# Optimization experiments

Hardware: AMD Instinct MI355X
Metric: run time of the kernel (lower is better)

Reference implementation:

```python
import jax, jax.numpy as jnp
import numpy as np

B, L, D, H = 2, 4096, 1024, 1  # head_dim == embed_dim in source, forcing H=1


def setup_inputs() -> dict:
    key = jax.random.key(0)
    k_x, kq, kk, kv, ko = jax.random.split(key, 5)
    s = 1.0 / np.sqrt(D)
    return {
        "x": jax.random.normal(k_x, (B, L, D), dtype=jnp.float32),
        "W_q": jax.random.normal(kq, (D, D), dtype=jnp.float32) * s,
        "W_k": jax.random.normal(kk, (D, D), dtype=jnp.float32) * s,
        "W_v": jax.random.normal(kv, (D, D), dtype=jnp.float32) * s,
        "W_o": jax.random.normal(ko, (D, D), dtype=jnp.float32) * s,
    }


def reference(x, W_q, W_k, W_v, W_o):
    # nn.Linear(y) = y @ W.T ; weights stored as (out, in)
    Hd = D  # head_dim = embed_dim (source quirk), so num_heads must be 1
    Q = jnp.einsum('bld,ed->ble', x, W_q).reshape(B, L, H, Hd).transpose(0, 2, 1, 3)
    K = jnp.einsum('bld,ed->ble', x, W_k).reshape(B, L, H, Hd).transpose(0, 2, 1, 3)
    V = jnp.einsum('bld,ed->ble', x, W_v).reshape(B, L, H, Hd).transpose(0, 2, 1, 3)
    scores = jnp.einsum('bhqd,bhkd->bhqk', Q, K) / jnp.sqrt(jnp.float32(Hd))
    attn = jax.nn.softmax(scores, axis=-1)
    out = jnp.einsum('bhqk,bhkd->bhqd', attn, V)  # (B,H,L,Hd)
    out = out.transpose(0, 2, 1, 3).reshape(B, L, D)
    return jnp.einsum('bld,ed->ble', out, W_o)
```

## Files before the change

### kernel.cpp

```cpp
#include <hip/hip_runtime.h>
#include <hip/hip_bf16.h>
#include <stdint.h>


typedef unsigned short u16;
typedef short short8 __attribute__((ext_vector_type(8)));
typedef float f32x4 __attribute__((ext_vector_type(4)));

__device__ __forceinline__ void async_ld16(void* lds, const void* g) {
  __builtin_amdgcn_global_load_lds(
      (const __attribute__((address_space(1))) unsigned int*)g,
      (__attribute__((address_space(3))) unsigned int*)lds,
      16, 0, 0);
}

__device__ __forceinline__ u16 f2bf(float f) {
  unsigned u = __float_as_uint(f);
  u += 0x7FFFu + ((u >> 16) & 1u);
  return (u16)(u >> 16);
}

__global__ __launch_bounds__(256)
void cast_f32_bf16(const float* __restrict__ in, u16* __restrict__ out, int n) {
  const int i = (blockIdx.x * 256 + threadIdx.x) * 8;
  if (i >= n) return;
  float4 a = ((const float4*)(in + i))[0];
  float4 b = ((const float4*)(in + i))[1];
  uint4 o;
  o.x = (unsigned)f2bf(a.x) | ((unsigned)f2bf(a.y) << 16);
  o.y = (unsigned)f2bf(a.z) | ((unsigned)f2bf(a.w) << 16);
  o.z = (unsigned)f2bf(b.x) | ((unsigned)f2bf(b.y) << 16);
  o.w = (unsigned)f2bf(b.z) | ((unsigned)f2bf(b.w) << 16);
  *(uint4*)(out + i) = o;
}

__global__ __launch_bounds__(256)
void cast_w4_bf16(const float* __restrict__ w0, const float* __restrict__ w1,
                  const float* __restrict__ w2, const float* __restrict__ w3,
                  u16* __restrict__ out) {
  const int idx = (blockIdx.x * 256 + threadIdx.x) * 8;
  const int which = idx >> 20;
  const int off = idx & 1048575;
  const float* src = which == 0 ? w0 : which == 1 ? w1 : which == 2 ? w2 : w3;
  float4 a = ((const float4*)(src + off))[0];
  float4 b = ((const float4*)(src + off))[1];
  uint4 o;
  o.x = (unsigned)f2bf(a.x) | ((unsigned)f2bf(a.y) << 16);
  o.y = (unsigned)f2bf(a.z) | ((unsigned)f2bf(a.w) << 16);
  o.z = (unsigned)f2bf(b.x) | ((unsigned)f2bf(b.y) << 16);
  o.w = (unsigned)f2bf(b.z) | ((unsigned)f2bf(b.w) << 16);
  *(uint4*)(out + idx) = o;
}

#define BM 128
#define BN 128
#define BK 32

template <int XSWZ>
__global__ __launch_bounds__(256)
void gemm_bt(const u16* __restrict__ A, const u16* __restrict__ Bt,
             void* __restrict__ Cv, int K, int lda, int ldb, int ldc,
             long long sAz, long long sBz, long long sCz,
             float scale, int store_f32) {
  __shared__ u16 As[3][BM * BK];
  __shared__ u16 Bs[3][BN * BK];

  int bx, by, bz;
  if constexpr (XSWZ) {
    const int gx = gridDim.x, gy = gridDim.y;
    const int nwg = gx * gy * gridDim.z;
    const int lin = (blockIdx.z * gy + blockIdx.y) * gx + blockIdx.x;
    const int chunk = nwg >> 3;
    const int swz = (lin & 7) * chunk + (lin >> 3);
    bx = swz % gx;
    const int t1 = swz / gx;
    by = t1 % gy;
    bz = t1 / gy;
  } else {
    bx = blockIdx.x; by = blockIdx.y; bz = blockIdx.z;
  }

  A  += (long long)bz * sAz;
  Bt += (long long)bz * sBz;

  const int tid  = threadIdx.x;
  const int wave = tid >> 6;
  const int lane = tid & 63;
  const int wm   = wave >> 1;
  const int wn   = wave & 1;
  const int r15  = lane & 15;
  const int q4   = lane >> 4;

  const int tileM = by * BM;
  const int tileN = bx * BN;

  const int srow = tid >> 2;
  const int scol = ((tid & 3) ^ (srow & 3)) * 8;

  const u16* Aptr = A + (long long)tileM * lda + scol;
  const u16* Bptr = Bt + (long long)tileN * ldb + scol;

  auto stage = [&](int kt) {
    const int b = kt % 3;
    const int k0 = kt * BK;
    u16* as = &As[b][tid * 8];
    u16* bs = &Bs[b][tid * 8];
    async_ld16(as,        Aptr + (long long)srow * lda + k0);
    async_ld16(as + 2048, Aptr + (long long)(srow + 64) * lda + k0);
    async_ld16(bs,        Bptr + (long long)srow * ldb + k0);
    async_ld16(bs + 2048, Bptr + (long long)(srow + 64) * ldb + k0);
  };

  f32x4 zero = {0.f, 0.f, 0.f, 0.f};
  f32x4 acc[4][4];
#pragma unroll
  for (int i = 0; i < 4; ++i)
#pragma unroll
    for (int j = 0; j < 4; ++j) acc[i][j] = zero;

  const int csw = ((q4 ^ (r15 & 3)) * 8);

  const int NT = K / BK;
  stage(0);
  if (NT > 1) stage(1);
  if (NT > 2) stage(2);

  for (int kt = 0; kt < NT; ++kt) {
    const int rem = NT - 1 - kt;
    if (rem >= 2)      asm volatile("s_waitcnt vmcnt(8)" ::: "memory");
    else if (rem == 1) asm volatile("s_waitcnt vmcnt(4)" ::: "memory");
    else               asm volatile("s_waitcnt vmcnt(0)" ::: "memory");
    __builtin_amdgcn_s_barrier();

    const int b = kt % 3;
    const u16* as = &As[b][0];
    const u16* bs = &Bs[b][0];

    short8 af[4], bf[4];
#pragma unroll
    for (int i = 0; i < 4; ++i)
      af[i] = *(const short8*)&as[(wm * 64 + i * 16 + r15) * BK + csw];
#pragma unroll
    for (int i = 0; i < 4; ++i)
      bf[i] = *(const short8*)&bs[(wn * 64 + i * 16 + r15) * BK + csw];

    __builtin_amdgcn_s_setprio(1);
#pragma unroll
    for (int i = 0; i < 4; ++i)
#pragma unroll
      for (int j = 0; j < 4; ++j)
        acc[i][j] = __builtin_amdgcn_mfma_f32_16x16x32_bf16(af[i], bf[j], acc[i][j], 0, 0, 0);
    __builtin_amdgcn_s_setprio(0);

    __builtin_amdgcn_s_barrier();
    if (kt + 3 < NT) stage(kt + 3);
  }

#pragma unroll
  for (int i = 0; i < 4; ++i) {
#pragma unroll
    for (int j = 0; j < 4; ++j) {
      const int col = tileN + wn * 64 + j * 16 + r15;
#pragma unroll
      for (int r = 0; r < 4; ++r) {
        const int row = tileM + wm * 64 + i * 16 + q4 * 4 + r;
        const long long idx = (long long)bz * sCz + (long long)row * ldc + col;
        const float val = acc[i][j][r] * scale;
        if (store_f32) ((float*)Cv)[idx] = val;
        else           ((u16*)Cv)[idx] = f2bf(val);
      }
    }
  }
}

__global__ __launch_bounds__(512, 2)
void gemm256_8ph(const u16* __restrict__ A, const u16* __restrict__ Bt,
                 u16* __restrict__ C, int K, int lda, int ldb, int ldc,
                 long long sAz, long long sBz, long long sCz, float scale) {
  __shared__ u16 smem[49152];

  const int gx = gridDim.x, gy = gridDim.y;
  const int nwg = gx * gy * gridDim.z;
  const int lin = (blockIdx.z * gy + blockIdx.y) * gx + blockIdx.x;
  const int chunk = nwg >> 3;
  const int swz = (lin & 7) * chunk + (lin >> 3);
  const int bx = swz % gx;
  const int t1 = swz / gx;
  const int by = t1 % gy;
  const int bz = t1 / gy;

  A  += (long long)bz * sAz;
  Bt += (long long)bz * sBz;
  const long long cbase = (long long)bz * sCz;

  const int tid  = threadIdx.x;
  const int wid  = tid >> 6;
  const int lane = tid & 63;
  const int wm   = wid >> 2;
  const int wn   = wid & 3;
  const int r15  = lane & 15;
  const int q4   = lane >> 4;

  const int tileM = by * 256;
  const int tileN = bx * 256;

  const int sr  = tid >> 2;
  const int gc8 = ((((tid & 3) - ((tid >> 3) & 3)) & 3)) * 8;

  const u16* Asrc = A  + (long long)(tileM + sr) * lda + gc8;
  const u16* Bsrc = Bt + (long long)(tileN + sr) * ldb + gc8;

  auto stage2A = [&](int kt) {
    u16* d = &smem[(kt % 3) * 16384 + tid * 8];
    async_ld16(d,        Asrc + kt * 32);
    async_ld16(d + 4096, Asrc + (long long)128 * lda + kt * 32);
  };
  auto stage2B = [&](int kt) {
    u16* d = &smem[(kt % 3) * 16384 + 8192 + tid * 8];
    async_ld16(d,        Bsrc + kt * 32);
    async_ld16(d + 4096, Bsrc + (long long)128 * ldb + kt * 32);
  };

  const int csw = (((q4 + (r15 >> 1)) & 3)) * 8;

  f32x4 acc[8][4];
#pragma unroll
  for (int i = 0; i < 8; ++i)
#pragma unroll
    for (int j = 0; j < 4; ++j) acc[i][j] = (f32x4){0.f, 0.f, 0.f, 0.f};

  const int NT = K >> 5;

  stage2A(0); stage2B(0);
  if (NT > 1) { stage2A(1); stage2B(1); }

  for (int t = 0; t < NT; ++t) {
    if (t + 1 < NT) asm volatile("s_waitcnt vmcnt(4)" ::: "memory");
    else            asm volatile("s_waitcnt vmcnt(0)" ::: "memory");
    __builtin_amdgcn_s_barrier();

    const u16* bufA = &smem[(t % 3) * 16384];
    const u16* bufB = bufA + 8192;

    short8 bf[4], af[4];
#pragma unroll
    for (int j = 0; j < 4; ++j)
      bf[j] = *(const short8*)&bufB[(wn * 64 + j * 16 + r15) * 32 + csw];
#pragma unroll
    for (int i = 0; i < 4; ++i)
      af[i] = *(const short8*)&bufA[(wm * 128 + i * 16 + r15) * 32 + csw];
    if (t + 2 < NT) stage2A(t + 2);
    __builtin_amdgcn_s_barrier();

    __builtin_amdgcn_s_setprio(1);
#pragma unroll
    for (int i = 0; i < 4; ++i)
#pragma unroll
      for (int j = 0; j < 4; ++j)
        acc[i][j] = __builtin_amdgcn_mfma_f32_16x16x32_bf16(af[i], bf[j], acc[i][j], 0, 0, 0);
    __builtin_amdgcn_s_setprio(0);
    __builtin_amdgcn_s_barrier();

#pragma unroll
    for (int i = 0; i < 4; ++i)
      af[i] = *(const short8*)&bufA[(wm * 128 + 64 + i * 16 + r15) * 32 + csw];
    if (t + 2 < NT) stage2B(t + 2);
    __builtin_amdgcn_s_barrier();

    __builtin_amdgcn_s_setprio(1);
#pragma unroll
    for (int i = 0; i < 4; ++i)
#pragma unroll
      for (int j = 0; j < 4; ++j)
        acc[4 + i][j] = __builtin_amdgcn_mfma_f32_16x16x32_bf16(af[i], bf[j], acc[4 + i][j], 0, 0, 0);
    __builtin_amdgcn_s_setprio(0);
    __builtin_amdgcn_s_barrier();
  }

  const int crow = tileM + wm * 128 + q4 * 4;
  const int ccol = tileN + wn * 64 + r15;
#pragma unroll
  for (int mi = 0; mi < 8; ++mi)
#pragma unroll
    for (int nj = 0; nj < 4; ++nj)
#pragma unroll
      for (int r = 0; r < 4; ++r) {
        const long long row = crow + mi * 16 + r;
        C[cbase + row * ldc + (ccol + nj * 16)] = f2bf(acc[mi][nj][r] * scale);
      }
}

__global__ __launch_bounds__(256)
void softmax_rows(u16* __restrict__ S) {
  const int tid = threadIdx.x;
  u16* rp = S + (long long)blockIdx.x * 4096;

  uint4 a = ((const uint4*)rp)[tid * 2];
  uint4 b = ((const uint4*)rp)[tid * 2 + 1];
  unsigned w[8] = {a.x, a.y, a.z, a.w, b.x, b.y, b.z, b.w};
  float v[16];
#pragma unroll
  for (int i = 0; i < 8; ++i) {
    v[2 * i]     = __uint_as_float(w[i] << 16);
    v[2 * i + 1] = __uint_as_float(w[i] & 0xFFFF0000u);
  }

  float m = v[0];
#pragma unroll
  for (int i = 1; i < 16; ++i) m = fmaxf(m, v[i]);
#pragma unroll
  for (int o = 32; o > 0; o >>= 1) m = fmaxf(m, __shfl_xor(m, o));
  __shared__ float redm[4];
  __shared__ float reds[4];
  const int wave = tid >> 6;
  if ((tid & 63) == 0) redm[wave] = m;
  __syncthreads();
  m = fmaxf(fmaxf(redm[0], redm[1]), fmaxf(redm[2], redm[3]));

  float s = 0.f;
#pragma unroll
  for (int i = 0; i < 16; ++i) {
    v[i] = __expf(v[i] - m);
    s += v[i];
  }
#pragma unroll
  for (int o = 32; o > 0; o >>= 1) s += __shfl_xor(s, o);
  if ((tid & 63) == 0) reds[wave] = s;
  __syncthreads();
  s = (reds[0] + reds[1]) + (reds[2] + reds[3]);
  const float inv = 1.0f / s;

#pragma unroll
  for (int i = 0; i < 8; ++i)
    w[i] = (unsigned)f2bf(v[2 * i] * inv) | ((unsigned)f2bf(v[2 * i + 1] * inv) << 16);
  uint4 oa = {w[0], w[1], w[2], w[3]};
  uint4 ob = {w[4], w[5], w[6], w[7]};
  ((uint4*)rp)[tid * 2] = oa;
  ((uint4*)rp)[tid * 2 + 1] = ob;
}

extern "C" void kernel_launch(void* const* d_in, const int* in_sizes, int n_in,
                              void* d_out, int out_size, void* d_ws, size_t ws_size,
                              hipStream_t stream) {
  const float* x  = (const float*)d_in[0];
  const float* Wq = (const float*)d_in[1];
  const float* Wk = (const float*)d_in[2];
  const float* Wv = (const float*)d_in[3];
  const float* Wo = (const float*)d_in[4];
  float* out = (float*)d_out;

  u16* xb  = (u16*)d_ws;
  u16* Wqb = xb  + 8388608;
  u16* Wkb = Wqb + 1048576;
  u16* Wvb = Wkb + 1048576;
  u16* Wob = Wvb + 1048576;
  u16* QKp = Wob + 1048576;
  u16* Vt  = QKp + 16777216;
  u16* S   = Vt  + 8388608;
  u16* O   = QKp;

  const dim3 blk(256);

  cast_f32_bf16<<<dim3(4096), blk, 0, stream>>>(x, xb, 8388608);
  cast_w4_bf16<<<dim3(2048), blk, 0, stream>>>(Wq, Wk, Wv, Wo, Wqb);

  gemm_bt<1><<<dim3(16, 64, 1), blk, 0, stream>>>(xb, Wqb, QKp,
                                                  1024, 1024, 1024, 2048,
                                                  0, 0, 0, 1.f, 0);
  gemm_bt<0><<<dim3(64, 8, 1), blk, 0, stream>>>(Wvb, xb, Vt,
                                                 1024, 1024, 1024, 8192,
                                                 0, 0, 0, 1.f, 0);
  gemm256_8ph<<<dim3(16, 16, 2), dim3(512), 0, stream>>>(
      QKp, QKp + 1024, S, 1024, 2048, 2048, 4096,
      8388608LL, 8388608LL, 16777216LL, 0.03125f);
  softmax_rows<<<dim3(8192), blk, 0, stream>>>(S);
  gemm_bt<1><<<dim3(8, 32, 2), blk, 0, stream>>>(S, Vt, O,
                                                 4096, 4096, 8192, 1024,
                                                 16777216LL, 4096LL, 4194304LL,
                                                 1.f, 0);
  gemm_bt<1><<<dim3(8, 64, 1), blk, 0, stream>>>(O, Wob, out,
                                                 1024, 1024, 1024, 1024,
                                                 0, 0, 0, 1.f, 1);
}
```

Baseline: 389.8 us.

## Fuse softmax normalization into PV GEMM using precomputed row max and inverse sum

The softmax kernel now only computes per-row max and inverse sum, stored as float2 in reused workspace. The exponentiation is applied to the score tiles inside a new PV GEMM kernel, and the inverse sum is applied at output. This removes the full write-back of the normalized probability matrix. In exchange, exp is recomputed redundantly for every N-tile inside the MFMA loop, which adds VALU work to the GEMM.

Result: slower. 483.1 us (+23.9%).

```diff
diff --git a/kernel.cpp b/kernel.cpp
--- a/kernel.cpp
+++ b/kernel.cpp
@@ -173,6 +173,149 @@
   }
 }
 
+__global__ __launch_bounds__(256)
+void pv_bt(const u16* __restrict__ A, const u16* __restrict__ Bt,
+           u16* __restrict__ C, const float2* __restrict__ minv,
+           int K, int lda, int ldb, int ldc,
+           long long sAz, long long sBz, long long sCz) {
+  __shared__ u16 As[3][BM * BK];
+  __shared__ u16 Bs[3][BN * BK];
+
+  const int gx = gridDim.x, gy = gridDim.y;
+  const int nwg = gx * gy * gridDim.z;
+  const int lin = (blockIdx.z * gy + blockIdx.y) * gx + blockIdx.x;
+  const int chunk = nwg >> 3;
+  const int swz = (lin & 7) * chunk + (lin >> 3);
+  const int bx = swz % gx;
+  const int t1 = swz / gx;
+  const int by = t1 % gy;
+  const int bz = t1 / gy;
+
+  A  += (long long)bz * sAz;
+  Bt += (long long)bz * sBz;
+
+  const int tid  = threadIdx.x;
+  const int wave = tid >> 6;
+  const int lane = tid & 63;
+  const int wm   = wave >> 1;
+  const int wn   = wave & 1;
+  const int r15  = lane & 15;
+  const int q4   = lane >> 4;
+
+  const int tileM = by * BM;
+  const int tileN = bx * BN;
+
+  const int srow = tid >> 2;
+  const int scol = ((tid & 3) ^ (srow & 3)) * 8;
+
+  const u16* Aptr = A + (long long)tileM * lda + scol;
+  const u16* Bptr = Bt + (long long)tileN * ldb + scol;
+
+  auto stage = [&](int kt) {
+    const int b = kt % 3;
+    const int k0 = kt * BK;
+    u16* as = &As[b][tid * 8];
+    u16* bs = &Bs[b][tid * 8];
+    async_ld16(as,        Aptr + (long long)srow * lda + k0);
+    async_ld16(as + 2048, Aptr + (long long)(srow + 64) * lda + k0);
+    async_ld16(bs,        Bptr + (long long)srow * ldb + k0);
+    async_ld16(bs + 2048, Bptr + (long long)(srow + 64) * ldb + k0);
+  };
+
+  const int rbase = bz * 4096 + tileM + wm * 64 + r15;
+  float am[4];
+#pragma unroll
+  for (int i = 0; i < 4; ++i) am[i] = minv[rbase + i * 16].x;
+
+  auto xf = [&](short8 v, float m) -> short8 {
+    union { short8 s; uint4 u; } in, out;
+    in.s = v;
+    unsigned w0 = in.u.x, w1 = in.u.y, w2 = in.u.z, w3 = in.u.w;
+    unsigned o0, o1, o2, o3;
+    {
+      float lo = __uint_as_float(w0 << 16), hi = __uint_as_float(w0 & 0xFFFF0000u);
+      o0 = (unsigned)f2bf(__expf(lo - m)) | ((unsigned)f2bf(__expf(hi - m)) << 16);
+    }
+    {
+      float lo = __uint_as_float(w1 << 16), hi = __uint_as_float(w1 & 0xFFFF0000u);
+      o1 = (unsigned)f2bf(__expf(lo - m)) | ((unsigned)f2bf(__expf(hi - m)) << 16);
+    }
+    {
+      float lo = __uint_as_float(w2 << 16), hi = __uint_as_float(w2 & 0xFFFF0000u);
+      o2 = (unsigned)f2bf(__expf(lo - m)) | ((unsigned)f2bf(__expf(hi - m)) << 16);
+    }
+    {
+      float lo = __uint_as_float(w3 << 16), hi = __uint_as_float(w3 & 0xFFFF0000u);
+      o3 = (unsigned)f2bf(__expf(lo - m)) | ((unsigned)f2bf(__expf(hi - m)) << 16);
+    }
+    out.u = make_uint4(o0, o1, o2, o3);
+    return out.s;
+  };
+
+  f32x4 zero = {0.f, 0.f, 0.f, 0.f};
+  f32x4 acc[4][4];
+#pragma unroll
+  for (int i = 0; i < 4; ++i)
+#pragma unroll
+    for (int j = 0; j < 4; ++j) acc[i][j] = zero;
+
+  const int csw = ((q4 ^ (r15 & 3)) * 8);
+
+  const int NT = K / BK;
+  stage(0);
+  if (NT > 1) stage(1);
+  if (NT > 2) stage(2);
+
+  for (int kt = 0; kt < NT; ++kt) {
+    const int rem = NT - 1 - kt;
+    if (rem >= 2)      asm volatile("s_waitcnt vmcnt(8)" ::: "memory");
+    else if (rem == 1) asm volatile("s_waitcnt vmcnt(4)" ::: "memory");
+    else               asm volatile("s_waitcnt vmcnt(0)" ::: "memory");
+    __builtin_amdgcn_s_barrier();
+
+    const int b = kt % 3;
+    const u16* as = &As[b][0];
+    const u16* bs = &Bs[b][0];
+
+    short8 af[4], bf[4];
+#pragma unroll
+    for (int i = 0; i < 4; ++i)
+      af[i] = *(const short8*)&as[(wm * 64 + i * 16 + r15) * BK + csw];
+#pragma unroll
+    for (int i = 0; i < 4; ++i)
+      bf[i] = *(const short8*)&bs[(wn * 64 + i * 16 + r15) * BK + csw];
+
+#pragma unroll
+    for (int i = 0; i < 4; ++i) af[i] = xf(af[i], am[i]);
+
+    __builtin_amdgcn_s_setprio(1);
+#pragma unroll
+    for (int i = 0; i < 4; ++i)
+#pragma unroll
+      for (int j = 0; j < 4; ++j)
+        acc[i][j] = __builtin_amdgcn_mfma_f32_16x16x32_bf16(af[i], bf[j], acc[i][j], 0, 0, 0);
+    __builtin_amdgcn_s_setprio(0);
+
+    __builtin_amdgcn_s_barrier();
+    if (kt + 3 < NT) stage(kt + 3);
+  }
+
+#pragma unroll
+  for (int i = 0; i < 4; ++i) {
+#pragma unroll
+    for (int j = 0; j < 4; ++j) {
+      const int col = tileN + wn * 64 + j * 16 + r15;
+#pragma unroll
+      for (int r = 0; r < 4; ++r) {
+        const int row = tileM + wm * 64 + i * 16 + q4 * 4 + r;
+        const float invs = minv[bz * 4096 + row].y;
+        const long long idx = (long long)bz * sCz + (long long)row * ldc + col;
+        C[idx] = f2bf(acc[i][j][r] * invs);
+      }
+    }
+  }
+}
+
 __global__ __launch_bounds__(512, 2)
 void gemm256_8ph(const u16* __restrict__ A, const u16* __restrict__ Bt,
                  u16* __restrict__ C, int K, int lda, int ldb, int ldc,
@@ -291,9 +434,9 @@
 }
 
 __global__ __launch_bounds__(256)
-void softmax_rows(u16* __restrict__ S) {
+void rowstat_rows(const u16* __restrict__ S, float2* __restrict__ minv) {
   const int tid = threadIdx.x;
-  u16* rp = S + (long long)blockIdx.x * 4096;
+  const u16* rp = S + (long long)blockIdx.x * 4096;
 
   uint4 a = ((const uint4*)rp)[tid * 2];
   uint4 b = ((const uint4*)rp)[tid * 2 + 1];
@@ -319,24 +462,14 @@
 
   float s = 0.f;
 #pragma unroll
-  for (int i = 0; i < 16; ++i) {
-    v[i] = __expf(v[i] - m);
-    s += v[i];
-  }
+  for (int i = 0; i < 16; ++i) s += __expf(v[i] - m);
 #pragma unroll
   for (int o = 32; o > 0; o >>= 1) s += __shfl_xor(s, o);
   if ((tid & 63) == 0) reds[wave] = s;
   __syncthreads();
   s = (reds[0] + reds[1]) + (reds[2] + reds[3]);
-  const float inv = 1.0f / s;
-
-#pragma unroll
-  for (int i = 0; i < 8; ++i)
-    w[i] = (unsigned)f2bf(v[2 * i] * inv) | ((unsigned)f2bf(v[2 * i + 1] * inv) << 16);
-  uint4 oa = {w[0], w[1], w[2], w[3]};
-  uint4 ob = {w[4], w[5], w[6], w[7]};
-  ((uint4*)rp)[tid * 2] = oa;
-  ((uint4*)rp)[tid * 2 + 1] = ob;
+
+  if (tid == 0) minv[blockIdx.x] = make_float2(m, 1.0f / s);
 }
 
 extern "C" void kernel_launch(void* const* d_in, const int* in_sizes, int n_in,
@@ -358,6 +491,7 @@
   u16* Vt  = QKp + 16777216;
   u16* S   = Vt  + 8388608;
   u16* O   = QKp;
+  float2* minv = (float2*)xb;
 
   const dim3 blk(256);
 
@@ -373,11 +507,10 @@
   gemm256_8ph<<<dim3(16, 16, 2), dim3(512), 0, stream>>>(
       QKp, QKp + 1024, S, 1024, 2048, 2048, 4096,
       8388608LL, 8388608LL, 16777216LL, 0.03125f);
-  softmax_rows<<<dim3(8192), blk, 0, stream>>>(S);
-  gemm_bt<1><<<dim3(8, 32, 2), blk, 0, stream>>>(S, Vt, O,
-                                                 4096, 4096, 8192, 1024,
-                                                 16777216LL, 4096LL, 4194304LL,
-                                                 1.f, 0);
+  rowstat_rows<<<dim3(8192), blk, 0, stream>>>(S, minv);
+  pv_bt<<<dim3(8, 32, 2), blk, 0, stream>>>(S, Vt, O, minv,
+                                            4096, 4096, 8192, 1024,
+                                            16777216LL, 4096LL, 4194304LL);
   gemm_bt<1><<<dim3(8, 64, 1), blk, 0, stream>>>(O, Wob, out,
                                                  1024, 1024, 1024, 1024,
                                                  0, 0, 0, 1.f, 1);
```
